# Kernel optimization log

Measured on AMD Instinct MI355X. Metric: run time of the kernel, lower is better.

Reference implementation:

```python
import jax, jax.numpy as jnp
import numpy as np

K = 3       # kernel size
PAD = 1     # dcn_pad
STRIDE = 1
DIL = 1     # dilation
GN_EPS = 1e-5


def _conv2d(x, w, b):
    # standard NCHW conv, stride 1, pad 1
    y = jax.lax.conv_general_dilated(
        x, w, (STRIDE, STRIDE), [(PAD, PAD), (PAD, PAD)],
        rhs_dilation=(DIL, DIL),
        dimension_numbers=('NCHW', 'OIHW', 'NCHW'))
    return y + b[None, :, None, None]


def _modulated_deform_conv(x, w_off, b_off, w, b):
    B, C, H, W = x.shape
    KK = K * K
    # offset/mask branch (ModulatedDeformConv2dPack.conv_offset)
    off = _conv2d(x, w_off, b_off)                     # [B, 3*KK, H, W]
    o1, o2, m = jnp.split(off, 3, axis=1)
    offset = jnp.concatenate([o1, o2], axis=1)         # [B, 2*KK, H, W]
    mask = jax.nn.sigmoid(m)                           # [B, KK, H, W]
    # channel 2k = dy, channel 2k+1 = dx for kernel tap k
    offset = offset.reshape(B, KK, 2, H, W)
    dy, dx = offset[:, :, 0], offset[:, :, 1]          # [B, KK, H, W]

    ki = jnp.arange(KK) // K                            # kernel row index
    kj = jnp.arange(KK) % K                             # kernel col index
    base_y = (jnp.arange(H)[None, :, None] - PAD + ki[:, None, None] * DIL)  # [KK,H,1]
    base_x = (jnp.arange(W)[None, None, :] - PAD + kj[:, None, None] * DIL)  # [KK,1,W]
    py = base_y.astype(x.dtype) + dy                   # [B, KK, H, W]
    px = base_x.astype(x.dtype) + dx

    y0f = jnp.floor(py); x0f = jnp.floor(px)
    ly = py - y0f; lx = px - x0f
    y0 = y0f.astype(jnp.int32); x0 = x0f.astype(jnp.int32)

    xf = x.reshape(B, C, H * W)

    def gather(yi, xi):
        # zero-padded gather at integer corner (yi, xi)
        valid = (yi >= 0) & (yi < H) & (xi >= 0) & (xi < W)
        idx = jnp.clip(yi, 0, H - 1) * W + jnp.clip(xi, 0, W - 1)  # [B,KK,H,W]
        g = jax.vmap(lambda xb, ib: jnp.take(xb, ib.reshape(-1), axis=1))(xf, idx)
        g = g.reshape(B, C, KK, H, W)
        return g * valid[:, None].astype(x.dtype)

    val = (gather(y0, x0)         * ((1 - ly) * (1 - lx))[:, None]
         + gather(y0, x0 + 1)     * ((1 - ly) * lx)[:, None]
         + gather(y0 + 1, x0)     * (ly * (1 - lx))[:, None]
         + gather(y0 + 1, x0 + 1) * (ly * lx)[:, None])     # [B,C,KK,H,W]
    val = val * mask[:, None]                                # modulation

    out = jnp.einsum('bckhw,ock->bohw', val, w.reshape(w.shape[0], C, KK))
    return out + b[None, :, None, None]


def _groupnorm1_relu(y, gamma, beta):
    # GroupNorm(num_groups=1): normalize over (C,H,W) per sample
    mu = y.mean(axis=(1, 2, 3), keepdims=True)
    var = y.var(axis=(1, 2, 3), keepdims=True)
    yn = (y - mu) * jax.lax.rsqrt(var + GN_EPS)
    return jax.nn.relu(yn * gamma[None, :, None, None] + beta[None, :, None, None])


def setup_inputs() -> dict:
    key = jax.random.key(0)
    ks = jax.random.split(key, 5)
    B, C, H, W = 4, 256, 64, 64
    CO = 256
    x = jax.random.normal(ks[0], (B, C, H, W), jnp.float32)
    w_off = jax.random.normal(ks[1], (3 * K * K, C, K, K), jnp.float32) * 0.01
    b_off = jax.random.normal(ks[2], (3 * K * K,), jnp.float32) * 0.01
    w = jax.random.normal(ks[3], (CO, C, K, K), jnp.float32) * (1.0 / np.sqrt(C * K * K))
    b = jax.random.normal(ks[4], (CO,), jnp.float32) * 0.01
    gamma = jnp.ones((CO,), jnp.float32)
    beta = jnp.zeros((CO,), jnp.float32)
    return dict(x=x, w_off=w_off, b_off=b_off, w=w, b=b, gamma=gamma, beta=beta)


def reference(x, w_off, b_off, w, b, gamma, beta):
    y = _modulated_deform_conv(x, w_off, b_off, w, b)
    return _groupnorm1_relu(y, gamma, beta)
```

## Files before the change

### kernel.cpp

```cpp
#include <hip/hip_runtime.h>

#define B_ 4
#define C_ 256
#define H_ 64
#define W_ 64
#define HW_ 4096
#define CO_ 256
#define NPX_ 16384
#define GN_EPS_ 1e-5f

typedef float f32x4 __attribute__((ext_vector_type(4)));
typedef short s16x8 __attribute__((ext_vector_type(8)));

__device__ __forceinline__ short f2bf(float f) {
    union { float f; unsigned u; } v; v.f = f;
    unsigned r = (v.u + 0x7FFFu + ((v.u >> 16) & 1u)) >> 16;
    return (short)(r & 0xFFFFu);
}
__device__ __forceinline__ float bf2f(short s) {
    union { unsigned u; float f; } v; v.u = ((unsigned)s & 0xFFFFu) << 16;
    return v.f;
}

__device__ __forceinline__ void gld_lds16(const void* g, void* l) {
    __builtin_amdgcn_global_load_lds(
        (const __attribute__((address_space(1))) unsigned*)g,
        (__attribute__((address_space(3))) unsigned*)l,
        16, 0, 0);
}

__global__ void k_prep_w(const float* __restrict__ w, short* __restrict__ wT) {
    int oc = blockIdx.x, c = threadIdx.x;
    const float* src = w + (oc * 256 + c) * 9;
    float v[9];
#pragma unroll
    for (int t = 0; t < 9; ++t) v[t] = src[t];
#pragma unroll
    for (int t = 0; t < 9; ++t) wT[(t * 256 + oc) * 256 + c] = f2bf(v[t]);
}

__global__ void k_prep_woff(const float* __restrict__ w_off, short* __restrict__ wOffT) {
    int o = blockIdx.x;
    int c = threadIdx.x;
    if (o < 27) {
        const float* src = w_off + (o * 256 + c) * 9;
#pragma unroll
        for (int t = 0; t < 9; ++t)
            wOffT[(t * 32 + o) * 256 + c] = f2bf(src[t]);
    } else {
#pragma unroll
        for (int t = 0; t < 9; ++t)
            wOffT[(t * 32 + o) * 256 + c] = 0;
    }
}

__global__ void k_xpose(const float* __restrict__ x, short* __restrict__ xT) {
    __shared__ short T[64 * 72];

    int bx  = blockIdx.x;
    int px0 = (bx & 255) * 64;
    int c0  = (bx >> 8) * 64;
    int b   = px0 >> 12;
    int hw0 = px0 & 4095;

    int t  = threadIdx.x;
    int cl = t & 63;
    int q  = t >> 6;

    const float4* src = reinterpret_cast<const float4*>(
        x + (long)(b * 256 + c0 + cl) * 4096 + hw0);
#pragma unroll
    for (int j = 0; j < 4; ++j) {
        float4 v = src[j * 4 + q];
        int pl = (j * 4 + q) * 4;
        T[(pl + 0) * 72 + cl] = f2bf(v.x);
        T[(pl + 1) * 72 + cl] = f2bf(v.y);
        T[(pl + 2) * 72 + cl] = f2bf(v.z);
        T[(pl + 3) * 72 + cl] = f2bf(v.w);
    }
    __syncthreads();

    int pl = t >> 2;
    int s  = t & 3;
    short* dst = xT + (long)(px0 + pl) * 256 + c0 + s * 16;
    s16x8 a    = *reinterpret_cast<const s16x8*>(&T[pl * 72 + s * 16]);
    s16x8 bseg = *reinterpret_cast<const s16x8*>(&T[pl * 72 + s * 16 + 8]);
    *reinterpret_cast<s16x8*>(dst)     = a;
    *reinterpret_cast<s16x8*>(dst + 8) = bseg;
}

__global__ __launch_bounds__(256, 4) void k_offmfma(
        const short* __restrict__ xT, const short* __restrict__ wOffT,
        float* __restrict__ offp) {
    int tid  = threadIdx.x;
    int lane = tid & 63;
    int wv   = tid >> 6;

    int px0  = blockIdx.x * 64 + wv * 16;
    int cc0  = blockIdx.y * 64;
    int lm   = lane & 15;
    int lk   = cc0 + (lane >> 4) * 8;

    int pxA = px0 + lm;
    int h   = (pxA >> 6) & 63;
    int w   = pxA & 63;

    f32x4 acc[2];
    acc[0] = (f32x4)0.f; acc[1] = (f32x4)0.f;

#pragma unroll
    for (int kk = 0; kk < 9; ++kk) {
        const int ki = kk / 3, kj = kk % 3;
        int hh = h + ki - 1, ww = w + kj - 1;
        bool valid = ((unsigned)hh < 64u) & ((unsigned)ww < 64u);
        int srcpx = valid ? (pxA + (ki - 1) * 64 + (kj - 1)) : 0;
        const short* aP = xT + (long)srcpx * 256 + lk;
        const short* bP = wOffT + (long)(kk * 32 + lm) * 256 + lk;
#pragma unroll
        for (int ks = 0; ks < 2; ++ks) {
            s16x8 a = *reinterpret_cast<const s16x8*>(aP + ks * 32);
            if (!valid) a = (s16x8)0;
            s16x8 b0 = *reinterpret_cast<const s16x8*>(bP + ks * 32);
            s16x8 b1 = *reinterpret_cast<const s16x8*>(bP + 16 * 256 + ks * 32);
            acc[0] = __builtin_amdgcn_mfma_f32_16x16x32_bf16(a, b0, acc[0], 0, 0, 0);
            acc[1] = __builtin_amdgcn_mfma_f32_16x16x32_bf16(a, b1, acc[1], 0, 0, 0);
        }
    }

    float* op = offp + (long)blockIdx.y * 27 * NPX_;
#pragma unroll
    for (int nt = 0; nt < 2; ++nt) {
        int oc = nt * 16 + lm;
        if (oc < 27) {
#pragma unroll
            for (int j = 0; j < 4; ++j) {
                int px = px0 + (lane >> 4) * 4 + j;
                op[oc * NPX_ + px] = acc[nt][j];
            }
        }
    }
}

__global__ void k_offreduce(const float* __restrict__ offp, const float* __restrict__ b_off,
                            float* __restrict__ off) {
    int idx = blockIdx.x * 256 + threadIdx.x;
    int oc  = idx >> 14;
    float s = b_off[oc];
#pragma unroll
    for (int j = 0; j < 4; ++j) s += offp[(long)j * 27 * NPX_ + idx];
    off[idx] = s;
}

__global__ __launch_bounds__(512, 1) void k_fused(
        const short* __restrict__ xT, const float* __restrict__ off,
        const short* __restrict__ wT, const float* __restrict__ bias,
        float* __restrict__ out, float* __restrict__ gnpart) {
    __shared__ __attribute__((aligned(16))) char lds[81920];
    __shared__ float red[16];

    int tid  = threadIdx.x;
    int lane = tid & 63;
    int wv   = tid >> 6;

    int px0 = blockIdx.x * 64;
    int b   = px0 >> 12;
    int hw0 = px0 & 4095;
    int h   = hw0 >> 6;
    long rb = (long)b * 4096;

    int spx = tid >> 3;
    int j8  = (tid & 7) * 8;
    int pg  = px0 + spx;
    int abyte = spx * 128 + (((tid & 7) << 4) ^ ((spx & 7) << 4));

    int brow_lane = lane >> 3;
    int bqg = (((lane & 7) ^ brow_lane) & 7) << 4;

    int wm = (wv & 1) * 32;
    int wn = (wv >> 1) * 64;
    int lm = lane & 15;
    int kq = lane >> 4;

    const char* wTb = (const char*)wT;

    f32x4 acc[2][4];
#pragma unroll
    for (int i = 0; i < 2; ++i)
#pragma unroll
        for (int j = 0; j < 4; ++j) acc[i][j] = (f32x4)0.f;

    float sw00 = 0.f, sw01 = 0.f, sw10 = 0.f, sw11 = 0.f;
    const short *p00 = xT, *p01 = xT, *p10 = xT, *p11 = xT;

#define STAGE_(t, buf)                                                               \
    {                                                                                \
        int kk_ = (t) >> 2, cq_ = (t) & 3;                                           \
        if (((t) & 3) == 0) {                                                        \
            int ki_ = kk_ / 3, kj_ = kk_ % 3;                                        \
            float dy = off[(2 * kk_) * NPX_ + pg];                                   \
            float dx = off[(2 * kk_ + 1) * NPX_ + pg];                               \
            float mk = off[(18 + kk_) * NPX_ + pg];                                  \
            mk = 1.f / (1.f + __expf(-mk));                                          \
            float py  = (float)(h + ki_ - 1) + dy;                                   \
            float pxf = (float)(spx + kj_ - 1) + dx;                                 \
            float y0f = floorf(py), x0f = floorf(pxf);                               \
            float ly = py - y0f, lx = pxf - x0f;                                     \
            int y0 = (int)y0f, x0 = (int)x0f;                                        \
            int y1 = y0 + 1, x1 = x0 + 1;                                            \
            sw00 = (1.f - ly) * (1.f - lx) * mk;                                     \
            sw01 = (1.f - ly) * lx * mk;                                             \
            sw10 = ly * (1.f - lx) * mk;                                             \
            sw11 = ly * lx * mk;                                                     \
            bool vy0 = (y0 >= 0) & (y0 < H_);                                        \
            bool vy1 = (y1 >= 0) & (y1 < H_);                                        \
            bool vx0 = (x0 >= 0) & (x0 < W_);                                        \
            bool vx1 = (x1 >= 0) & (x1 < W_);                                        \
            if (!(vy0 & vx0)) sw00 = 0.f;                                            \
            if (!(vy0 & vx1)) sw01 = 0.f;                                            \
            if (!(vy1 & vx0)) sw10 = 0.f;                                            \
            if (!(vy1 & vx1)) sw11 = 0.f;                                            \
            int cy0 = min(max(y0, 0), H_ - 1), cy1 = min(max(y1, 0), H_ - 1);        \
            int cx0 = min(max(x0, 0), W_ - 1), cx1 = min(max(x1, 0), W_ - 1);        \
            p00 = xT + (rb + cy0 * 64 + cx0) * 256;                                  \
            p01 = xT + (rb + cy0 * 64 + cx1) * 256;                                  \
            p10 = xT + (rb + cy1 * 64 + cx0) * 256;                                  \
            p11 = xT + (rb + cy1 * 64 + cx1) * 256;                                  \
        }                                                                            \
        _Pragma("unroll")                                                            \
        for (int g = 0; g < 4; ++g) {                                                \
            int row8 = wv * 4 + g;                         \
            int ocr  = row8 * 8 + brow_lane;                                         \
            const char* srcB = wTb + ((long)(kk_ * 256 + ocr) << 9)                  \
                               + cq_ * 128 + bqg;                                    \
            gld_lds16(srcB, (void*)(lds + (buf) * 40960 + 8192 + row8 * 1024));      \
        }                                                                            \
        int coff = cq_ * 64 + j8;                                                    \
        s16x8 r00 = *reinterpret_cast<const s16x8*>(p00 + coff);                     \
        s16x8 r01 = *reinterpret_cast<const s16x8*>(p01 + coff);                     \
        s16x8 r10 = *reinterpret_cast<const s16x8*>(p10 + coff);                     \
        s16x8 r11 = *reinterpret_cast<const s16x8*>(p11 + coff);                     \
        s16x8 o8;                                                                    \
        _Pragma("unroll")                                                            \
        for (int jj = 0; jj < 8; ++jj) {                                             \
            float g2 = sw00 * bf2f(r00[jj]) + sw01 * bf2f(r01[jj])                   \
                     + sw10 * bf2f(r10[jj]) + sw11 * bf2f(r11[jj]);                  \
            o8[jj] = f2bf(g2);                                                       \
        }                                                                            \
        *reinterpret_cast<s16x8*>(lds + (buf) * 40960 + abyte) = o8;                 \
    }

#define COMPUTE_(buf)                                                                \
    {                                                                                \
        const char* Ab = lds + (buf) * 40960;                                        \
        const char* Bb = lds + (buf) * 40960 + 8192;                                 \
        _Pragma("unroll")                                                            \
        for (int ksub = 0; ksub < 2; ++ksub) {                                       \
            int cb_ = ksub * 64 + kq * 16;                                           \
            s16x8 a[2], bfr[4];                                                      \
            _Pragma("unroll")                                                        \
            for (int mf = 0; mf < 2; ++mf) {                                         \
                int pl_ = wm + mf * 16 + lm;                                         \
                a[mf] = *reinterpret_cast<const s16x8*>(                             \
                    Ab + pl_ * 128 + (cb_ ^ ((pl_ & 7) << 4)));                      \
            }                                                                        \
            _Pragma("unroll")                                                        \
            for (int nf = 0; nf < 4; ++nf) {                                         \
                int ol_ = wn + nf * 16 + lm;                                         \
                bfr[nf] = *reinterpret_cast<const s16x8*>(                           \
                    Bb + ol_ * 128 + (cb_ ^ ((ol_ & 7) << 4)));                      \
            }                                                                        \
            _Pragma("unroll")                                                        \
            for (int mf = 0; mf < 2; ++mf)                                           \
                _Pragma("unroll")                                                    \
                for (int nf = 0; nf < 4; ++nf)                                       \
                    acc[mf][nf] = __builtin_amdgcn_mfma_f32_16x16x32_bf16(           \
                        a[mf], bfr[nf], acc[mf][nf], 0, 0, 0);                       \
        }                                                                            \
    }

    STAGE_(0, 0);
    __syncthreads();

    int cur = 0;
#pragma unroll 1
    for (int t = 0; t < 36; ++t) {
        if (t < 35) STAGE_(t + 1, cur ^ 1);
        COMPUTE_(cur);
        __syncthreads();
        cur ^= 1;
    }
#undef STAGE_
#undef COMPUTE_

    float s = 0.f, sq = 0.f;
#pragma unroll
    for (int nf = 0; nf < 4; ++nf) {
        int oc = wn + nf * 16 + lm;
        float bv = bias[oc];
        float* orow = out + (b * CO_ + oc) * HW_ + hw0 + wm;
#pragma unroll
        for (int mf = 0; mf < 2; ++mf) {
            f32x4 r = acc[mf][nf];
            r.x += bv; r.y += bv; r.z += bv; r.w += bv;
            s  += r.x + r.y + r.z + r.w;
            sq += r.x * r.x + r.y * r.y + r.z * r.z + r.w * r.w;
            *reinterpret_cast<f32x4*>(orow + mf * 16 + kq * 4) = r;
        }
    }
#pragma unroll
    for (int o = 32; o > 0; o >>= 1) {
        s  += __shfl_down(s, o, 64);
        sq += __shfl_down(sq, o, 64);
    }
    if (lane == 0) { red[wv * 2] = s; red[wv * 2 + 1] = sq; }
    __syncthreads();
    if (tid == 0) {
        float S = 0.f, SQ = 0.f;
#pragma unroll
        for (int k = 0; k < 8; ++k) { S += red[k * 2]; SQ += red[k * 2 + 1]; }
        gnpart[blockIdx.x * 2]     = S;
        gnpart[blockIdx.x * 2 + 1] = SQ;
    }
}

__global__ void k_gn_stats(const float* __restrict__ part, float* __restrict__ stats) {
    int b = blockIdx.x, t = threadIdx.x;
    float2 v = reinterpret_cast<const float2*>(part)[b * 64 + t];
    float s = v.x, sq = v.y;
#pragma unroll
    for (int o = 32; o > 0; o >>= 1) {
        s  += __shfl_down(s, o, 64);
        sq += __shfl_down(sq, o, 64);
    }
    if (t == 0) {
        const float n = (float)(CO_ * HW_);
        float mean = s / n;
        float var  = sq / n - mean * mean;
        stats[b * 2] = mean;
        stats[b * 2 + 1] = rsqrtf(var + GN_EPS_);
    }
}

__global__ void k_gn_apply(float* __restrict__ y, const float* __restrict__ stats,
                           const float* __restrict__ gamma, const float* __restrict__ beta) {
    int e4 = blockIdx.x * 256 + threadIdx.x;
    int b  = e4 >> 18;
    int oc = (e4 >> 10) & 255;
    float mean = stats[b * 2], rstd = stats[b * 2 + 1];
    float g  = gamma[oc] * rstd;
    float bb = beta[oc] - mean * g;
    float4* p = reinterpret_cast<float4*>(y);
    float4 v = p[e4];
    v.x = fmaxf(v.x * g + bb, 0.f);
    v.y = fmaxf(v.y * g + bb, 0.f);
    v.z = fmaxf(v.z * g + bb, 0.f);
    v.w = fmaxf(v.w * g + bb, 0.f);
    p[e4] = v;
}

extern "C" void kernel_launch(void* const* d_in, const int* in_sizes, int n_in,
                              void* d_out, int out_size, void* d_ws, size_t ws_size,
                              hipStream_t stream) {
    const float* x     = (const float*)d_in[0];
    const float* w_off = (const float*)d_in[1];
    const float* b_off = (const float*)d_in[2];
    const float* w     = (const float*)d_in[3];
    const float* bias  = (const float*)d_in[4];
    const float* gamma = (const float*)d_in[5];
    const float* beta  = (const float*)d_in[6];
    float* out = (float*)d_out;

    float* Wp     = (float*)d_ws;
    float* off    = Wp;
    short* wT     = (short*)(off + 27 * NPX_);
    short* wOffT  = wT + 9 * 256 * 256;
    float* gnpart = (float*)(wOffT + 9 * 32 * 256);
    float* stats  = gnpart + 512;
    short* xT     = (short*)(stats + 8);
    float* offp   = (float*)(xT + (long)NPX_ * 256);

    k_prep_w<<<256, 256, 0, stream>>>(w, wT);
    k_prep_woff<<<32, 256, 0, stream>>>(w_off, wOffT);
    k_xpose<<<1024, 256, 0, stream>>>(x, xT);
    k_offmfma<<<dim3(256, 4), 256, 0, stream>>>(xT, wOffT, offp);
    k_offreduce<<<1728, 256, 0, stream>>>(offp, b_off, off);
    k_fused<<<256, 512, 0, stream>>>(xT, off, wT, bias, out, gnpart);
    k_gn_stats<<<4, 64, 0, stream>>>(gnpart, stats);
    k_gn_apply<<<4096, 256, 0, stream>>>(out, stats, gamma, beta);
}
```

Baseline: 178.9 us.

## Halve K-chunk size, split stage into issue/write, raise occupancy of fused deform GEMM

Shrinks each K-step from 64 to 32 channels, halving LDS to 40 KB so the launch bounds can request up to 4 blocks per CU instead of 1. The gather stage is split into an issue phase (global loads and async weight copies) placed before the MFMA compute and a write phase (bilinear blend and LDS store) placed after it, so load latency overlaps with compute. Only half the threads do the gather, with a new 4-way XOR swizzle. The cost is twice as many loop iterations and barriers, fewer MFMAs per barrier, and tighter register limits that may cause spills.

New measurement: 196.3 us. 1.1x slower.

```diff
diff --git a/kernel.cpp b/kernel.cpp
--- a/kernel.cpp
+++ b/kernel.cpp
@@ -151,11 +151,11 @@
     off[idx] = s;
 }
 
-__global__ __launch_bounds__(512, 1) void k_fused(
+__global__ __launch_bounds__(512, 4) void k_fused(
         const short* __restrict__ xT, const float* __restrict__ off,
         const short* __restrict__ wT, const float* __restrict__ bias,
         float* __restrict__ out, float* __restrict__ gnpart) {
-    __shared__ __attribute__((aligned(16))) char lds[81920];
+    __shared__ __attribute__((aligned(16))) char lds[40960];
     __shared__ float red[16];
 
     int tid  = threadIdx.x;
@@ -168,13 +168,13 @@
     int h   = hw0 >> 6;
     long rb = (long)b * 4096;
 
-    int spx = tid >> 3;
-    int j8  = (tid & 7) * 8;
+    int spx = tid >> 2;
+    int oct = tid & 3;
     int pg  = px0 + spx;
-    int abyte = spx * 128 + (((tid & 7) << 4) ^ ((spx & 7) << 4));
-
-    int brow_lane = lane >> 3;
-    int bqg = (((lane & 7) ^ brow_lane) & 7) << 4;
+    int abyte_w = spx * 64 + ((oct ^ ((spx >> 1) & 3)) << 4);
+
+    int brow = lane >> 2;
+    int bq   = lane & 3;
 
     int wm = (wv & 1) * 32;
     int wn = (wv >> 1) * 64;
@@ -191,11 +191,12 @@
 
     float sw00 = 0.f, sw01 = 0.f, sw10 = 0.f, sw11 = 0.f;
     const short *p00 = xT, *p01 = xT, *p10 = xT, *p11 = xT;
-
-#define STAGE_(t, buf)                                                               \
+    s16x8 r00, r01, r10, r11;
+
+#define ISSUE_(tt, buf)                                                              \
     {                                                                                \
-        int kk_ = (t) >> 2, cq_ = (t) & 3;                                           \
-        if (((t) & 3) == 0) {                                                        \
+        int kk_ = (tt) >> 3, cq_ = (tt) & 7;                                         \
+        if ((((tt) & 7) == 0) && tid < 256) {                                        \
             int ki_ = kk_ / 3, kj_ = kk_ % 3;                                        \
             float dy = off[(2 * kk_) * NPX_ + pg];                                   \
             float dx = off[(2 * kk_ + 1) * NPX_ + pg];                               \
@@ -226,19 +227,26 @@
             p10 = xT + (rb + cy1 * 64 + cx0) * 256;                                  \
             p11 = xT + (rb + cy1 * 64 + cx1) * 256;                                  \
         }                                                                            \
-        _Pragma("unroll")                                                            \
-        for (int g = 0; g < 4; ++g) {                                                \
-            int row8 = wv * 4 + g;                         \
-            int ocr  = row8 * 8 + brow_lane;                                         \
-            const char* srcB = wTb + ((long)(kk_ * 256 + ocr) << 9)                  \
-                               + cq_ * 128 + bqg;                                    \
-            gld_lds16(srcB, (void*)(lds + (buf) * 40960 + 8192 + row8 * 1024));      \
-        }                                                                            \
-        int coff = cq_ * 64 + j8;                                                    \
-        s16x8 r00 = *reinterpret_cast<const s16x8*>(p00 + coff);                     \
-        s16x8 r01 = *reinterpret_cast<const s16x8*>(p01 + coff);                     \
-        s16x8 r10 = *reinterpret_cast<const s16x8*>(p10 + coff);                     \
-        s16x8 r11 = *reinterpret_cast<const s16x8*>(p11 + coff);                     \
+        if (tid < 256) {                                                             \
+            int coff = cq_ * 32 + oct * 8;                                           \
+            r00 = *reinterpret_cast<const s16x8*>(p00 + coff);                       \
+            r01 = *reinterpret_cast<const s16x8*>(p01 + coff);                       \
+            r10 = *reinterpret_cast<const s16x8*>(p10 + coff);                       \
+            r11 = *reinterpret_cast<const s16x8*>(p11 + coff);                       \
+        }                                                                            \
+        _Pragma("unroll")                                                            \
+        for (int g = 0; g < 2; ++g) {                                                \
+            int row = wv * 32 + g * 16 + brow;                                       \
+            int qs  = bq ^ ((row >> 1) & 3);                                         \
+            const char* srcB = wTb + ((long)(kk_ * 256 + row)) * 512                 \
+                               + cq_ * 64 + qs * 16;                                 \
+            gld_lds16(srcB, (void*)(lds + (buf) * 20480 + 4096                       \
+                                    + (wv * 32 + g * 16) * 64));                     \
+        }                                                                            \
+    }
+
+#define WRITE_(buf)                                                                  \
+    if (tid < 256) {                                                                 \
         s16x8 o8;                                                                    \
         _Pragma("unroll")                                                            \
         for (int jj = 0; jj < 8; ++jj) {                                             \
@@ -246,50 +254,49 @@
                      + sw10 * bf2f(r10[jj]) + sw11 * bf2f(r11[jj]);                  \
             o8[jj] = f2bf(g2);                                                       \
         }                                                                            \
-        *reinterpret_cast<s16x8*>(lds + (buf) * 40960 + abyte) = o8;                 \
+        *reinterpret_cast<s16x8*>(lds + (buf) * 20480 + abyte_w) = o8;               \
     }
 
 #define COMPUTE_(buf)                                                                \
     {                                                                                \
-        const char* Ab = lds + (buf) * 40960;                                        \
-        const char* Bb = lds + (buf) * 40960 + 8192;                                 \
-        _Pragma("unroll")                                                            \
-        for (int ksub = 0; ksub < 2; ++ksub) {                                       \
-            int cb_ = ksub * 64 + kq * 16;                                           \
-            s16x8 a[2], bfr[4];                                                      \
+        const char* Ab = lds + (buf) * 20480;                                        \
+        const char* Bb = Ab + 4096;                                                  \
+        s16x8 a[2], bfr[4];                                                          \
+        _Pragma("unroll")                                                            \
+        for (int mf = 0; mf < 2; ++mf) {                                             \
+            int pl_ = wm + mf * 16 + lm;                                             \
+            a[mf] = *reinterpret_cast<const s16x8*>(                                 \
+                Ab + pl_ * 64 + ((kq ^ ((pl_ >> 1) & 3)) << 4));                     \
+        }                                                                            \
+        _Pragma("unroll")                                                            \
+        for (int nf = 0; nf < 4; ++nf) {                                             \
+            int ol_ = wn + nf * 16 + lm;                                             \
+            bfr[nf] = *reinterpret_cast<const s16x8*>(                               \
+                Bb + ol_ * 64 + ((kq ^ ((ol_ >> 1) & 3)) << 4));                     \
+        }                                                                            \
+        _Pragma("unroll")                                                            \
+        for (int mf = 0; mf < 2; ++mf)                                               \
             _Pragma("unroll")                                                        \
-            for (int mf = 0; mf < 2; ++mf) {                                         \
-                int pl_ = wm + mf * 16 + lm;                                         \
-                a[mf] = *reinterpret_cast<const s16x8*>(                             \
-                    Ab + pl_ * 128 + (cb_ ^ ((pl_ & 7) << 4)));                      \
-            }                                                                        \
-            _Pragma("unroll")                                                        \
-            for (int nf = 0; nf < 4; ++nf) {                                         \
-                int ol_ = wn + nf * 16 + lm;                                         \
-                bfr[nf] = *reinterpret_cast<const s16x8*>(                           \
-                    Bb + ol_ * 128 + (cb_ ^ ((ol_ & 7) << 4)));                      \
-            }                                                                        \
-            _Pragma("unroll")                                                        \
-            for (int mf = 0; mf < 2; ++mf)                                           \
-                _Pragma("unroll")                                                    \
-                for (int nf = 0; nf < 4; ++nf)                                       \
-                    acc[mf][nf] = __builtin_amdgcn_mfma_f32_16x16x32_bf16(           \
-                        a[mf], bfr[nf], acc[mf][nf], 0, 0, 0);                       \
-        }                                                                            \
-    }
-
-    STAGE_(0, 0);
+            for (int nf = 0; nf < 4; ++nf)                                           \
+                acc[mf][nf] = __builtin_amdgcn_mfma_f32_16x16x32_bf16(               \
+                    a[mf], bfr[nf], acc[mf][nf], 0, 0, 0);                           \
+    }
+
+    ISSUE_(0, 0);
+    WRITE_(0);
     __syncthreads();
 
     int cur = 0;
 #pragma unroll 1
-    for (int t = 0; t < 36; ++t) {
-        if (t < 35) STAGE_(t + 1, cur ^ 1);
+    for (int t = 0; t < 72; ++t) {
+        if (t < 71) ISSUE_(t + 1, cur ^ 1);
         COMPUTE_(cur);
+        if (t < 71) WRITE_(cur ^ 1);
         __syncthreads();
         cur ^= 1;
     }
-#undef STAGE_
+#undef ISSUE_
+#undef WRITE_
 #undef COMPUTE_
 
     float s = 0.f, sq = 0.f;
```
